# Optimization experiments

Measured on AMD Instinct MI355X. Metric: run time of the kernel, lower is better.

The kernel has to match this reference:

```python
import jax, jax.numpy as jnp
import numpy as np
import math

N_EMBD = 2048
N_HEAD = 16
HEAD_DIM = N_EMBD // N_HEAD  # 128
K = 8
P = 2
B = 1
T = 2048
EPS = 1e-6


def _rms_norm(x):
    return x * jax.lax.rsqrt(jnp.mean(x * x, axis=-1, keepdims=True) + EPS)


def _rope(x, cos, sin):
    # x: [B, T, H, D]; cos/sin: [T, D//2]
    d = x.shape[-1] // 2
    x1, x2 = x[..., :d], x[..., d:]
    c = cos[None, :, None, :]
    s = sin[None, :, None, :]
    return jnp.concatenate([x1 * c + x2 * s, -x1 * s + x2 * c], axis=-1)


def setup_inputs() -> dict:
    key = jax.random.key(0)
    ks = jax.random.split(key, 8)
    x = jax.random.normal(ks[0], (B, T, N_EMBD), jnp.float32)
    half = HEAD_DIM // 2
    inv_freq = 1.0 / (10000.0 ** (np.arange(half, dtype=np.float32) / half))
    ang = np.arange(T, dtype=np.float32)[:, None] * inv_freq[None, :]
    cos = jnp.asarray(np.cos(ang), jnp.float32)
    sin = jnp.asarray(np.sin(ang), jnp.float32)
    sc = 1.0 / math.sqrt(N_EMBD)
    Wq = jax.random.normal(ks[1], (N_EMBD, N_EMBD), jnp.float32) * sc
    Wk = jax.random.normal(ks[2], (N_EMBD, N_EMBD), jnp.float32) * sc
    Wv = jax.random.normal(ks[3], (N_EMBD, N_EMBD), jnp.float32) * sc
    Wproj = jax.random.normal(ks[4], (N_EMBD, N_EMBD), jnp.float32) * sc
    scd = 1.0 / math.sqrt(HEAD_DIM)
    Wdq = jax.random.normal(ks[5], (K, HEAD_DIM), jnp.float32) * scd
    Wdk = jax.random.normal(ks[6], (K, HEAD_DIM), jnp.float32) * scd
    return {"x": x, "cos": cos, "sin": sin, "Wq": Wq, "Wk": Wk, "Wv": Wv, "Wproj": Wproj, "Wdq": Wdq, "Wdk": Wdk}


def reference(x, cos, sin, Wq, Wk, Wv, Wproj, Wdq, Wdk):
    Bq, Tq, C = x.shape
    q = (x @ Wq.T).reshape(Bq, Tq, N_HEAD, HEAD_DIM)
    k = (x @ Wk.T).reshape(Bq, Tq, N_HEAD, HEAD_DIM)
    v = (x @ Wv.T).reshape(Bq, Tq, N_HEAD, HEAD_DIM)
    q = _rms_norm(_rope(q, cos, sin))
    k = _rms_norm(_rope(k, cos, sin))
    q = jnp.swapaxes(q, 1, 2)  # [B,H,T,D]
    k = jnp.swapaxes(k, 1, 2)
    v = jnp.swapaxes(v, 1, 2)
    # base-p digits in {0..p-1}; p=2 -> bits
    qd = jnp.floor(jax.nn.sigmoid(jnp.einsum('bhtd,kd->bhtk', q, Wdq)) * (P - 0.01)).astype(jnp.int32)
    kd = jnp.floor(jax.nn.sigmoid(jnp.einsum('bhtd,kd->bhtk', k, Wdk)) * (P - 0.01)).astype(jnp.int32)
    # lcp >= K-1  <=>  first K-1 digits all equal; pack them into one code
    pw = (P ** jnp.arange(K - 1)).astype(jnp.int32)  # [K-1]
    qc = jnp.sum(qd[..., : K - 1] * pw, axis=-1)  # [B,H,T]
    kc = jnp.sum(kd[..., : K - 1] * pw, axis=-1)
    lcp_mask = qc[..., :, None] == kc[..., None, :]  # [B,H,Tq,Tk]
    causal = jnp.tril(jnp.ones((Tq, Tq), dtype=bool))
    mask = lcp_mask & causal
    scores = jnp.einsum('bhqd,bhkd->bhqk', q, k) * (1.0 / math.sqrt(HEAD_DIM))
    s = jnp.where(mask, scores, -1e30)
    w = jax.nn.softmax(s, axis=-1)
    w = jnp.where(mask, w, 0.0)
    any_valid = jnp.any(mask, axis=-1, keepdims=True)
    w = jnp.where(any_valid, w, 0.0)  # fully-masked rows -> zero output (torch gives NaN)
    y = jnp.einsum('bhqk,bhkd->bhqd', w, v)
    y = jnp.swapaxes(y, 1, 2).reshape(Bq, Tq, C)
    return y @ Wproj.T
```

## Files before the change

### kernel.cpp

```cpp
#include <hip/hip_runtime.h>
#include <hip/hip_bf16.h>
#include <math.h>

#define T 2048
#define C 2048
#define NH 16
#define HD 128
#define SCALE 0.08838834764831845f
#define WL_CAP 2048
#define MARG 1e-4f

typedef short s16x8 __attribute__((ext_vector_type(8)));
typedef float f32x4 __attribute__((ext_vector_type(4)));
typedef _Float16 f16;
typedef f16 f16x8 __attribute__((ext_vector_type(8)));

__device__ __forceinline__ float wave_sum(float v) {
  #pragma unroll
  for (int o = 32; o > 0; o >>= 1) v += __shfl_xor(v, o, 64);
  return v;
}
__device__ __forceinline__ unsigned short f2bf(float f) {
  unsigned u = __float_as_uint(f);
  u += 0x7FFFu + ((u >> 16) & 1u);
  return (unsigned short)(u >> 16);
}

__global__ __launch_bounds__(256) void to_bf16(const float* __restrict__ in,
                                               unsigned short* __restrict__ outp,
                                               int n4) {
  int i = blockIdx.x * blockDim.x + threadIdx.x;
  const int stride = gridDim.x * blockDim.x;
  for (; i < n4; i += stride) {
    float4 v = ((const float4*)in)[i];
    ushort4 o;
    o.x = f2bf(v.x); o.y = f2bf(v.y); o.z = f2bf(v.z); o.w = f2bf(v.w);
    ((ushort4*)outp)[i] = o;
  }
}

#define PRESC 4096.0f
#define S0F 5.9604644775390625e-8f
#define S1F 2.9103830456733704e-11f
#define S2F 1.4210854715202004e-14f

__global__ __launch_bounds__(256) void split_f16(const float* __restrict__ in,
                                                 unsigned short* __restrict__ hip_,
                                                 unsigned short* __restrict__ lop,
                                                 int n4) {
  int i = blockIdx.x * blockDim.x + threadIdx.x;
  const int stride = gridDim.x * blockDim.x;
  for (; i < n4; i += stride) {
    float4 v = ((const float4*)in)[i];
    float s0 = v.x * PRESC, s1 = v.y * PRESC, s2 = v.z * PRESC, s3 = v.w * PRESC;
    union { f16 h[4]; ushort4 u; } H, L;
    H.h[0] = (f16)s0; H.h[1] = (f16)s1; H.h[2] = (f16)s2; H.h[3] = (f16)s3;
    L.h[0] = (f16)((s0 - (float)H.h[0]) * 2048.0f);
    L.h[1] = (f16)((s1 - (float)H.h[1]) * 2048.0f);
    L.h[2] = (f16)((s2 - (float)H.h[2]) * 2048.0f);
    L.h[3] = (f16)((s3 - (float)H.h[3]) * 2048.0f);
    ((ushort4*)hip_)[i] = H.u;
    ((ushort4*)lop)[i] = L.u;
  }
}

#define SBM 64
#define SBN 128
#define SBK 32

__global__ __launch_bounds__(256, 3) void gemm_qk_pre(const unsigned short* __restrict__ Ahp,
                                                      const unsigned short* __restrict__ Alp,
                                                      const unsigned short* __restrict__ Bhp,
                                                      const unsigned short* __restrict__ Blp,
                                                      float* __restrict__ Cc) {
  __shared__ unsigned short Ah[2][SBM * SBK];
  __shared__ unsigned short Av[2][SBM * SBK];
  __shared__ unsigned short Bh[2][SBN * SBK];
  __shared__ unsigned short Bv[2][SBN * SBK];
  const int tid = threadIdx.x;
  const int bm = blockIdx.x * SBM;
  const int bn = blockIdx.y * SBN;
  const int wv = tid >> 6, lane = tid & 63;
  const int wm = wv & 1, wn = wv >> 1;
  const int lrow = lane & 15, lquad = lane >> 4;

  const int a_row = tid >> 2, qg = tid & 3;
  const int a_qs = qg ^ ((a_row >> 1) & 3);
  const int b_row0 = tid >> 2;
  const int b_qs = qg ^ ((b_row0 >> 1) & 3);

  f32x4 acc[2][2][4];
  #pragma unroll
  for (int g = 0; g < 2; ++g)
    #pragma unroll
    for (int i = 0; i < 2; ++i)
      #pragma unroll
      for (int j = 0; j < 4; ++j) acc[g][i][j] = (f32x4){0.f, 0.f, 0.f, 0.f};

  {
    uint4 aH = *(const uint4*)(Ahp + (size_t)(bm + a_row) * C + qg * 8);
    uint4 aL = *(const uint4*)(Alp + (size_t)(bm + a_row) * C + qg * 8);
    uint4 b0H = *(const uint4*)(Bhp + (size_t)(bn + b_row0) * C + qg * 8);
    uint4 b0L = *(const uint4*)(Blp + (size_t)(bn + b_row0) * C + qg * 8);
    uint4 b1H = *(const uint4*)(Bhp + (size_t)(bn + 64 + b_row0) * C + qg * 8);
    uint4 b1L = *(const uint4*)(Blp + (size_t)(bn + 64 + b_row0) * C + qg * 8);
    *(uint4*)&Ah[0][a_row * SBK + a_qs * 8] = aH;
    *(uint4*)&Av[0][a_row * SBK + a_qs * 8] = aL;
    *(uint4*)&Bh[0][b_row0 * SBK + b_qs * 8] = b0H;
    *(uint4*)&Bv[0][b_row0 * SBK + b_qs * 8] = b0L;
    *(uint4*)&Bh[0][(64 + b_row0) * SBK + b_qs * 8] = b1H;
    *(uint4*)&Bv[0][(64 + b_row0) * SBK + b_qs * 8] = b1L;
  }
  __syncthreads();

  const int niter = C / SBK;
  for (int it = 0; it < niter; ++it) {
    const int cur = it & 1;
    const bool has = (it + 1) < niter;
    uint4 aHn, aLn, b0Hn, b0Ln, b1Hn, b1Ln;
    if (has) {
      const int k0 = (it + 1) * SBK;
      aHn = *(const uint4*)(Ahp + (size_t)(bm + a_row) * C + k0 + qg * 8);
      aLn = *(const uint4*)(Alp + (size_t)(bm + a_row) * C + k0 + qg * 8);
      b0Hn = *(const uint4*)(Bhp + (size_t)(bn + b_row0) * C + k0 + qg * 8);
      b0Ln = *(const uint4*)(Blp + (size_t)(bn + b_row0) * C + k0 + qg * 8);
      b1Hn = *(const uint4*)(Bhp + (size_t)(bn + 64 + b_row0) * C + k0 + qg * 8);
      b1Ln = *(const uint4*)(Blp + (size_t)(bn + 64 + b_row0) * C + k0 + qg * 8);
    }
    f16x8 ah[2], av[2], bh[4], bv[4];
    #pragma unroll
    for (int mi = 0; mi < 2; ++mi) {
      const int r = wm * 32 + mi * 16 + lrow;
      const int q = lquad ^ ((r >> 1) & 3);
      ah[mi] = *(const f16x8*)&Ah[cur][r * SBK + q * 8];
      av[mi] = *(const f16x8*)&Av[cur][r * SBK + q * 8];
    }
    #pragma unroll
    for (int ni = 0; ni < 4; ++ni) {
      const int r = wn * 64 + ni * 16 + lrow;
      const int q = lquad ^ ((r >> 1) & 3);
      bh[ni] = *(const f16x8*)&Bh[cur][r * SBK + q * 8];
      bv[ni] = *(const f16x8*)&Bv[cur][r * SBK + q * 8];
    }
    #pragma unroll
    for (int mi = 0; mi < 2; ++mi)
      #pragma unroll
      for (int ni = 0; ni < 4; ++ni) {
        acc[0][mi][ni] = __builtin_amdgcn_mfma_f32_16x16x32_f16(ah[mi], bh[ni], acc[0][mi][ni], 0, 0, 0);
        acc[1][mi][ni] = __builtin_amdgcn_mfma_f32_16x16x32_f16(ah[mi], bv[ni], acc[1][mi][ni], 0, 0, 0);
        acc[1][mi][ni] = __builtin_amdgcn_mfma_f32_16x16x32_f16(av[mi], bh[ni], acc[1][mi][ni], 0, 0, 0);
      }
    if (has) {
      const int nxt = cur ^ 1;
      *(uint4*)&Ah[nxt][a_row * SBK + a_qs * 8] = aHn;
      *(uint4*)&Av[nxt][a_row * SBK + a_qs * 8] = aLn;
      *(uint4*)&Bh[nxt][b_row0 * SBK + b_qs * 8] = b0Hn;
      *(uint4*)&Bv[nxt][b_row0 * SBK + b_qs * 8] = b0Ln;
      *(uint4*)&Bh[nxt][(64 + b_row0) * SBK + b_qs * 8] = b1Hn;
      *(uint4*)&Bv[nxt][(64 + b_row0) * SBK + b_qs * 8] = b1Ln;
    }
    __syncthreads();
  }
  #pragma unroll
  for (int mi = 0; mi < 2; ++mi)
    #pragma unroll
    for (int ni = 0; ni < 4; ++ni)
      #pragma unroll
      for (int r = 0; r < 4; ++r) {
        int row = bm + wm * 32 + mi * 16 + lquad * 4 + r;
        int col = bn + wn * 64 + ni * 16 + lrow;
        Cc[(size_t)row * C + col] = acc[0][mi][ni][r] * S0F + acc[1][mi][ni][r] * S1F;
      }
}

__device__ __forceinline__ void split8(const float4 v0, const float4 v1,
                                       uint4& hi, uint4& lo) {
  float s[8] = {v0.x * PRESC, v0.y * PRESC, v0.z * PRESC, v0.w * PRESC,
                v1.x * PRESC, v1.y * PRESC, v1.z * PRESC, v1.w * PRESC};
  union { uint4 u; f16 h[8]; } H, L;
  #pragma unroll
  for (int i = 0; i < 8; ++i) {
    f16 h2 = (f16)s[i];
    float d = s[i] - (float)h2;
    H.h[i] = h2;
    L.h[i] = (f16)(d * 2048.0f);
  }
  hi = H.u; lo = L.u;
}

__global__ __launch_bounds__(256, 2) void gemm_qk_split16(const float* __restrict__ A,
                                                          const float* __restrict__ Wq,
                                                          const float* __restrict__ Wk,
                                                          float* __restrict__ Qo,
                                                          float* __restrict__ Ko) {
  const float* __restrict__ Bw = blockIdx.z ? Wk : Wq;
  float* __restrict__ Cc = blockIdx.z ? Ko : Qo;
  __shared__ unsigned short Ah[2][SBM * SBK];
  __shared__ unsigned short Av[2][SBM * SBK];
  __shared__ unsigned short Bh[2][SBN * SBK];
  __shared__ unsigned short Bv[2][SBN * SBK];
  const int tid = threadIdx.x;
  const int bm = blockIdx.x * SBM;
  const int bn = blockIdx.y * SBN;
  const int wv = tid >> 6, lane = tid & 63;
  const int wm = wv & 1, wn = wv >> 1;
  const int lrow = lane & 15, lquad = lane >> 4;

  const int a_row = tid >> 2, qg = tid & 3;
  const int a_qs = qg ^ ((a_row >> 1) & 3);
  const int b_row0 = tid >> 2;
  const int b_qs = qg ^ ((b_row0 >> 1) & 3);

  f32x4 acc[3][2][4];
  #pragma unroll
  for (int g = 0; g < 3; ++g)
    #pragma unroll
    for (int i = 0; i < 2; ++i)
      #pragma unroll
      for (int j = 0; j < 4; ++j) acc[g][i][j] = (f32x4){0.f, 0.f, 0.f, 0.f};

  {
    const float* pA  = A  + (size_t)(bm + a_row) * C + qg * 8;
    const float* pB0 = Bw + (size_t)(bn + b_row0) * C + qg * 8;
    const float* pB1 = Bw + (size_t)(bn + 64 + b_row0) * C + qg * 8;
    uint4 h, l;
    split8(*(const float4*)pA, *(const float4*)(pA + 4), h, l);
    *(uint4*)&Ah[0][a_row * SBK + a_qs * 8] = h;
    *(uint4*)&Av[0][a_row * SBK + a_qs * 8] = l;
    split8(*(const float4*)pB0, *(const float4*)(pB0 + 4), h, l);
    *(uint4*)&Bh[0][b_row0 * SBK + b_qs * 8] = h;
    *(uint4*)&Bv[0][b_row0 * SBK + b_qs * 8] = l;
    split8(*(const float4*)pB1, *(const float4*)(pB1 + 4), h, l);
    *(uint4*)&Bh[0][(64 + b_row0) * SBK + b_qs * 8] = h;
    *(uint4*)&Bv[0][(64 + b_row0) * SBK + b_qs * 8] = l;
  }
  __syncthreads();

  const int niter = C / SBK;
  for (int it = 0; it < niter; ++it) {
    const int cur = it & 1;
    const bool has = (it + 1) < niter;
    float4 a0n, a1n, b00n, b01n, b10n, b11n;
    if (has) {
      const int k0 = (it + 1) * SBK;
      const float* pA  = A  + (size_t)(bm + a_row) * C + k0 + qg * 8;
      const float* pB0 = Bw + (size_t)(bn + b_row0) * C + k0 + qg * 8;
      const float* pB1 = Bw + (size_t)(bn + 64 + b_row0) * C + k0 + qg * 8;
      a0n = *(const float4*)pA;   a1n = *(const float4*)(pA + 4);
      b00n = *(const float4*)pB0; b01n = *(const float4*)(pB0 + 4);
      b10n = *(const float4*)pB1; b11n = *(const float4*)(pB1 + 4);
    }
    f16x8 ah[2], av[2], bh[4], bv[4];
    #pragma unroll
    for (int mi = 0; mi < 2; ++mi) {
      const int r = wm * 32 + mi * 16 + lrow;
      const int q = lquad ^ ((r >> 1) & 3);
      ah[mi] = *(const f16x8*)&Ah[cur][r * SBK + q * 8];
      av[mi] = *(const f16x8*)&Av[cur][r * SBK + q * 8];
    }
    #pragma unroll
    for (int ni = 0; ni < 4; ++ni) {
      const int r = wn * 64 + ni * 16 + lrow;
      const int q = lquad ^ ((r >> 1) & 3);
      bh[ni] = *(const f16x8*)&Bh[cur][r * SBK + q * 8];
      bv[ni] = *(const f16x8*)&Bv[cur][r * SBK + q * 8];
    }
    #pragma unroll
    for (int mi = 0; mi < 2; ++mi)
      #pragma unroll
      for (int ni = 0; ni < 4; ++ni) {
        acc[0][mi][ni] = __builtin_amdgcn_mfma_f32_16x16x32_f16(ah[mi], bh[ni], acc[0][mi][ni], 0, 0, 0);
        acc[1][mi][ni] = __builtin_amdgcn_mfma_f32_16x16x32_f16(ah[mi], bv[ni], acc[1][mi][ni], 0, 0, 0);
        acc[1][mi][ni] = __builtin_amdgcn_mfma_f32_16x16x32_f16(av[mi], bh[ni], acc[1][mi][ni], 0, 0, 0);
        acc[2][mi][ni] = __builtin_amdgcn_mfma_f32_16x16x32_f16(av[mi], bv[ni], acc[2][mi][ni], 0, 0, 0);
      }
    if (has) {
      const int nxt = cur ^ 1;
      uint4 h, l;
      split8(a0n, a1n, h, l);
      *(uint4*)&Ah[nxt][a_row * SBK + a_qs * 8] = h;
      *(uint4*)&Av[nxt][a_row * SBK + a_qs * 8] = l;
      split8(b00n, b01n, h, l);
      *(uint4*)&Bh[nxt][b_row0 * SBK + b_qs * 8] = h;
      *(uint4*)&Bv[nxt][b_row0 * SBK + b_qs * 8] = l;
      split8(b10n, b11n, h, l);
      *(uint4*)&Bh[nxt][(64 + b_row0) * SBK + b_qs * 8] = h;
      *(uint4*)&Bv[nxt][(64 + b_row0) * SBK + b_qs * 8] = l;
    }
    __syncthreads();
  }
  #pragma unroll
  for (int mi = 0; mi < 2; ++mi)
    #pragma unroll
    for (int ni = 0; ni < 4; ++ni)
      #pragma unroll
      for (int r = 0; r < 4; ++r) {
        int row = bm + wm * 32 + mi * 16 + lquad * 4 + r;
        int col = bn + wn * 64 + ni * 16 + lrow;
        float v = acc[0][mi][ni][r] * S0F + (acc[1][mi][ni][r] * S1F + acc[2][mi][ni][r] * S2F);
        Cc[(size_t)row * C + col] = v;
      }
}

#define VBM 64
#define VBN 128
#define VBK 32

__global__ __launch_bounds__(256) void gemm_bf16n(const unsigned short* __restrict__ A,
                                                  const unsigned short* __restrict__ B,
                                                  float* __restrict__ Cc) {
  __shared__ unsigned short Al[2][VBM * VBK];
  __shared__ unsigned short Bl[2][VBN * VBK];
  const int tid = threadIdx.x;
  const int bm = blockIdx.x * VBM;
  const int bn = blockIdx.y * VBN;
  const int wv = tid >> 6, lane = tid & 63;
  const int wm = wv & 1, wn = wv >> 1;
  const int lrow = lane & 15, lquad = lane >> 4;

  const int a_row = tid >> 2, qg = tid & 3;
  const int a_qs = qg ^ ((a_row >> 1) & 3);
  const int b_row0 = tid >> 2;
  const int b_qs = qg ^ ((b_row0 >> 1) & 3);

  f32x4 acc[2][4];
  #pragma unroll
  for (int i = 0; i < 2; ++i)
    #pragma unroll
    for (int j = 0; j < 4; ++j) acc[i][j] = (f32x4){0.f, 0.f, 0.f, 0.f};

  {
    uint4 av = *(const uint4*)(A + (size_t)(bm + a_row) * C + qg * 8);
    uint4 b0 = *(const uint4*)(B + (size_t)(bn + b_row0) * C + qg * 8);
    uint4 b1 = *(const uint4*)(B + (size_t)(bn + 64 + b_row0) * C + qg * 8);
    *(uint4*)&Al[0][a_row * VBK + a_qs * 8] = av;
    *(uint4*)&Bl[0][b_row0 * VBK + b_qs * 8] = b0;
    *(uint4*)&Bl[0][(64 + b_row0) * VBK + b_qs * 8] = b1;
  }
  __syncthreads();

  const int niter = C / VBK;
  for (int it = 0; it < niter; ++it) {
    const int cur = it & 1;
    const bool has = (it + 1) < niter;
    uint4 avn, b0n, b1n;
    if (has) {
      const int k0 = (it + 1) * VBK;
      avn = *(const uint4*)(A + (size_t)(bm + a_row) * C + k0 + qg * 8);
      b0n = *(const uint4*)(B + (size_t)(bn + b_row0) * C + k0 + qg * 8);
      b1n = *(const uint4*)(B + (size_t)(bn + 64 + b_row0) * C + k0 + qg * 8);
    }
    s16x8 af[2], bfr[4];
    #pragma unroll
    for (int mi = 0; mi < 2; ++mi) {
      const int r = wm * 32 + mi * 16 + lrow;
      const int q = lquad ^ ((r >> 1) & 3);
      af[mi] = *(const s16x8*)&Al[cur][r * VBK + q * 8];
    }
    #pragma unroll
    for (int ni = 0; ni < 4; ++ni) {
      const int r = wn * 64 + ni * 16 + lrow;
      const int q = lquad ^ ((r >> 1) & 3);
      bfr[ni] = *(const s16x8*)&Bl[cur][r * VBK + q * 8];
    }
    #pragma unroll
    for (int mi = 0; mi < 2; ++mi)
      #pragma unroll
      for (int ni = 0; ni < 4; ++ni)
        acc[mi][ni] = __builtin_amdgcn_mfma_f32_16x16x32_bf16(af[mi], bfr[ni], acc[mi][ni], 0, 0, 0);
    if (has) {
      const int nxt = cur ^ 1;
      *(uint4*)&Al[nxt][a_row * VBK + a_qs * 8] = avn;
      *(uint4*)&Bl[nxt][b_row0 * VBK + b_qs * 8] = b0n;
      *(uint4*)&Bl[nxt][(64 + b_row0) * VBK + b_qs * 8] = b1n;
    }
    __syncthreads();
  }
  #pragma unroll
  for (int mi = 0; mi < 2; ++mi)
    #pragma unroll
    for (int ni = 0; ni < 4; ++ni)
      #pragma unroll
      for (int r = 0; r < 4; ++r) {
        int row = bm + wm * 32 + mi * 16 + lquad * 4 + r;
        int col = bn + wn * 64 + ni * 16 + lrow;
        Cc[(size_t)row * C + col] = acc[mi][ni][r];
      }
}

__global__ void zero_ctr(int* __restrict__ ctr) {
  if (threadIdx.x == 0) ctr[0] = 0;
}

__global__ __launch_bounds__(256) void rope_fused(float* __restrict__ Qb,
                                                  float* __restrict__ Kb,
                                                  const float* __restrict__ cosb,
                                                  const float* __restrict__ sinb,
                                                  const float* __restrict__ Wdq,
                                                  const float* __restrict__ Wdk,
                                                  int* __restrict__ qcodes,
                                                  int* __restrict__ kcodes,
                                                  int* __restrict__ wl,
                                                  int* __restrict__ ctr) {
  float* __restrict__ buf = blockIdx.y ? Kb : Qb;
  const float* __restrict__ Wd = blockIdx.y ? Wdk : Wdq;
  int* __restrict__ codes = blockIdx.y ? kcodes : qcodes;
  int wave = (blockIdx.x << 2) + (threadIdx.x >> 6);
  int lane = threadIdx.x & 63;
  int t = wave / NH, h = wave % NH;
  size_t base = (size_t)t * C + h * HD;
  float x1 = buf[base + lane];
  float x2 = buf[base + lane + 64];
  float c = cosb[t * 64 + lane];
  float s = sinb[t * 64 + lane];
  float r1 = x1 * c + x2 * s;
  float r2 = x2 * c - x1 * s;
  float ss = wave_sum(r1 * r1 + r2 * r2);
  float inv = 1.0f / sqrtf(ss * (1.0f / 128.0f) + 1e-6f);
  r1 *= inv; r2 *= inv;
  buf[base + lane] = r1;
  buf[base + lane + 64] = r2;
  int code = 0;
  bool marg = false;
  #pragma unroll
  for (int kk = 0; kk < 7; ++kk) {
    float z = r1 * Wd[kk * HD + lane] + r2 * Wd[kk * HD + lane + 64];
    z = wave_sum(z);
    float sig = 1.0f / (1.0f + expf(-z));
    float d = sig * 1.99f - 1.0f;
    if (d >= 0.f) code |= (1 << kk);
    marg |= (fabsf(d) < MARG);
  }
  if (lane == 0) {
    codes[h * T + t] = code;
    if (marg) {
      int i = atomicAdd(ctr, 1);
      if (i < WL_CAP) wl[i] = ((int)blockIdx.y << 15) | (h << 11) | t;
    }
  }
}

__global__ __launch_bounds__(64) void fix_codes(const float* __restrict__ x,
                                                const float* __restrict__ Wq,
                                                const float* __restrict__ Wk,
                                                const float* __restrict__ cosb,
                                                const float* __restrict__ sinb,
                                                const float* __restrict__ Wdq,
                                                const float* __restrict__ Wdk,
                                                int* __restrict__ qc,
                                                int* __restrict__ kc,
                                                const int* __restrict__ wl,
                                                const int* __restrict__ ctr) {
  const int n = min(ctr[0], WL_CAP);
  const int lane = threadIdx.x;
  for (int e = blockIdx.x; e < n; e += gridDim.x) {
    const int ent = wl[e];
    const int isK = ent >> 15;
    const int h = (ent >> 11) & 15;
    const int t = ent & 2047;
    const float* __restrict__ W  = isK ? Wk : Wq;
    const float* __restrict__ Wd = isK ? Wdk : Wdq;
    int* __restrict__ codes = isK ? kc : qc;

    const float* xr = x + (size_t)t * C;
    const float* w0 = W + (size_t)(h * HD + lane) * C;
    const float* w1 = W + (size_t)(h * HD + lane + 64) * C;
    float p0[4] = {0.f, 0.f, 0.f, 0.f};
    float p1[4] = {0.f, 0.f, 0.f, 0.f};
    for (int k = 0; k < C; k += 4) {
      float4 xv = *(const float4*)(xr + k);
      float4 a = *(const float4*)(w0 + k);
      float4 b = *(const float4*)(w1 + k);
      p0[0] += xv.x * a.x; p0[1] += xv.y * a.y;
      p0[2] += xv.z * a.z; p0[3] += xv.w * a.w;
      p1[0] += xv.x * b.x; p1[1] += xv.y * b.y;
      p1[2] += xv.z * b.z; p1[3] += xv.w * b.w;
    }
    float x1 = (p0[0] + p0[1]) + (p0[2] + p0[3]);
    float x2 = (p1[0] + p1[1]) + (p1[2] + p1[3]);
    float c = cosb[t * 64 + lane];
    float s = sinb[t * 64 + lane];
    float r1 = x1 * c + x2 * s;
    float r2 = x2 * c - x1 * s;
    float ss = wave_sum(r1 * r1 + r2 * r2);
    float inv = 1.0f / sqrtf(ss * (1.0f / 128.0f) + 1e-6f);
    r1 *= inv; r2 *= inv;
    int code = 0;
    #pragma unroll
    for (int kk = 0; kk < 7; ++kk) {
      float z = r1 * Wd[kk * HD + lane] + r2 * Wd[kk * HD + lane + 64];
      z = wave_sum(z);
      float sig = 1.0f / (1.0f + expf(-z));
      if (sig * 1.99f >= 1.0f) code |= (1 << kk);
    }
    if (lane == 0) codes[h * T + t] = code;
  }
}

__global__ __launch_bounds__(256) void attn_sparse(const float* __restrict__ Q,
                                                   const float* __restrict__ Kn,
                                                   const float* __restrict__ V,
                                                   const int* __restrict__ qc,
                                                   const int* __restrict__ kc,
                                                   float* __restrict__ Y) {
  const int tid = threadIdx.x;
  const int lane = tid & 63;
  const int wave_id = blockIdx.x * 4 + (tid >> 6);
  const int h = wave_id & (NH - 1);
  const int qrow = wave_id >> 4;
  const size_t hb = (size_t)h * HD;

  const float q0 = Q[(size_t)qrow * C + hb + lane];
  const float q1 = Q[(size_t)qrow * C + hb + lane + 64];
  const int qcode = qc[h * T + qrow];
  const int* kch = kc + h * T;

  float m = -1e30f, l = 0.f, acc0 = 0.f, acc1 = 0.f;

  const int nchunks = (qrow >> 6) + 1;
  int kcj = kch[lane];
  for (int ci = 0; ci < nchunks; ++ci) {
    const int j0 = ci << 6;
    const int cur = kcj;
    if (ci + 1 < nchunks) kcj = kch[j0 + 64 + lane];
    unsigned long long mask = __ballot((cur == qcode) && (j0 + lane <= qrow));
    while (mask) {
      const int j = j0 + (__ffsll((long long)mask) - 1);
      mask &= mask - 1;
      const float* kr = Kn + (size_t)j * C + hb;
      const float* vr = V + (size_t)j * C + hb;
      const float k0v = kr[lane], k1v = kr[lane + 64];
      const float v0 = vr[lane], v1 = vr[lane + 64];
      const float s = wave_sum(q0 * k0v + q1 * k1v) * SCALE;
      const float m_new = fmaxf(m, s);
      const float alpha = __expf(m - m_new);
      const float p = __expf(s - m_new);
      l = l * alpha + p;
      acc0 = acc0 * alpha + p * v0;
      acc1 = acc1 * alpha + p * v1;
      m = m_new;
    }
  }
  const float invl = (l > 0.f) ? 1.0f / l : 0.f;
  Y[(size_t)qrow * C + hb + lane] = acc0 * invl;
  Y[(size_t)qrow * C + hb + lane + 64] = acc1 * invl;
}

extern "C" void kernel_launch(void* const* d_in, const int* in_sizes, int n_in,
                              void* d_out, int out_size, void* d_ws, size_t ws_size,
                              hipStream_t stream) {
  (void)in_sizes; (void)n_in; (void)out_size;
  const float* x     = (const float*)d_in[0];
  const float* cosb  = (const float*)d_in[1];
  const float* sinb  = (const float*)d_in[2];
  const float* Wq    = (const float*)d_in[3];
  const float* Wk    = (const float*)d_in[4];
  const float* Wv    = (const float*)d_in[5];
  const float* Wproj = (const float*)d_in[6];
  const float* Wdq   = (const float*)d_in[7];
  const float* Wdk   = (const float*)d_in[8];
  float* out = (float*)d_out;

  const size_t MB = 1024 * 1024;
  char* ws = (char*)d_ws;
  float* Kbuf = (float*)ws;
  float* V    = (float*)(ws + 16 * MB);
  float* Y    = (float*)(ws + 32 * MB);
  unsigned short* Wbf = (unsigned short*)(ws + 48 * MB);
  unsigned short* xbf = (unsigned short*)Y;
  unsigned short* Ybf = (unsigned short*)Kbuf;
  float* Q    = out;

  const int n4 = T * C / 4;

  if (ws_size >= (size_t)64 * MB) {
    unsigned short* xh  = (unsigned short*)Y;
    unsigned short* xl  = xh + (size_t)T * C;
    unsigned short* wqh = (unsigned short*)Kbuf;
    unsigned short* wql = wqh + (size_t)T * C;
    unsigned short* wkh = Wbf;
    unsigned short* wkl = (unsigned short*)(ws + 56 * MB);
    int* qc  = (int*)Wbf;
    int* kc  = qc + NH * T;
    int* ctr = kc + NH * T;
    int* wl  = ctr + 16;

    to_bf16<<<2048, 256, 0, stream>>>(x, xbf, n4);
    to_bf16<<<2048, 256, 0, stream>>>(Wv, Wbf, n4);
    gemm_bf16n<<<dim3(T / VBM, C / VBN), 256, 0, stream>>>(xbf, Wbf, V);
    split_f16<<<2048, 256, 0, stream>>>(x, xh, xl, n4);
    split_f16<<<2048, 256, 0, stream>>>(Wq, wqh, wql, n4);
    split_f16<<<2048, 256, 0, stream>>>(Wk, wkh, wkl, n4);
    gemm_qk_pre<<<dim3(T / SBM, C / SBN), 256, 0, stream>>>(xh, xl, wqh, wql, Q);
    gemm_qk_pre<<<dim3(T / SBM, C / SBN), 256, 0, stream>>>(xh, xl, wkh, wkl, Kbuf);
    zero_ctr<<<1, 64, 0, stream>>>(ctr);
    rope_fused<<<dim3(T * NH / 4, 2), 256, 0, stream>>>(Q, Kbuf, cosb, sinb, Wdq, Wdk, qc, kc, wl, ctr);
    fix_codes<<<256, 64, 0, stream>>>(x, Wq, Wk, cosb, sinb, Wdq, Wdk, qc, kc, wl, ctr);
    attn_sparse<<<T * NH / 4, 256, 0, stream>>>(Q, Kbuf, V, qc, kc, Y);
    to_bf16<<<2048, 256, 0, stream>>>(Y, Ybf, n4);
    to_bf16<<<2048, 256, 0, stream>>>(Wproj, Wbf, n4);
    gemm_bf16n<<<dim3(T / VBM, C / VBN), 256, 0, stream>>>(Ybf, Wbf, out);
  } else {
    int* qc  = (int*)(Wbf + (size_t)T * C);
    int* kc  = qc + NH * T;
    int* ctr = kc + NH * T;
    int* wl  = ctr + 16;

    to_bf16<<<2048, 256, 0, stream>>>(x, xbf, n4);
    to_bf16<<<2048, 256, 0, stream>>>(Wv, Wbf, n4);
    gemm_bf16n<<<dim3(T / VBM, C / VBN), 256, 0, stream>>>(xbf, Wbf, V);
    gemm_qk_split16<<<dim3(T / SBM, C / SBN, 2), 256, 0, stream>>>(x, Wq, Wk, Q, Kbuf);
    zero_ctr<<<1, 64, 0, stream>>>(ctr);
    rope_fused<<<dim3(T * NH / 4, 2), 256, 0, stream>>>(Q, Kbuf, cosb, sinb, Wdq, Wdk, qc, kc, wl, ctr);
    fix_codes<<<256, 64, 0, stream>>>(x, Wq, Wk, cosb, sinb, Wdq, Wdk, qc, kc, wl, ctr);
    attn_sparse<<<T * NH / 4, 256, 0, stream>>>(Q, Kbuf, V, qc, kc, Y);
    to_bf16<<<2048, 256, 0, stream>>>(Y, Ybf, n4);
    to_bf16<<<2048, 256, 0, stream>>>(Wproj, Wbf, n4);
    gemm_bf16n<<<dim3(T / VBM, C / VBN), 256, 0, stream>>>(Ybf, Wbf, out);
  }
}
```

Before: 504.4 us.

## Merge Q/K split GEMMs into one launch and reuse f16 x for V and proj GEMMs

```diff
diff --git a/kernel.cpp b/kernel.cpp
--- a/kernel.cpp
+++ b/kernel.cpp
@@ -64,15 +64,37 @@
   }
 }
 
+__global__ __launch_bounds__(256) void to_f16h(const float* __restrict__ in,
+                                               unsigned short* __restrict__ outp,
+                                               int n4) {
+  int i = blockIdx.x * blockDim.x + threadIdx.x;
+  const int stride = gridDim.x * blockDim.x;
+  for (; i < n4; i += stride) {
+    float4 v = ((const float4*)in)[i];
+    union { f16 h[4]; ushort4 u; } H;
+    H.h[0] = (f16)(v.x * PRESC); H.h[1] = (f16)(v.y * PRESC);
+    H.h[2] = (f16)(v.z * PRESC); H.h[3] = (f16)(v.w * PRESC);
+    ((ushort4*)outp)[i] = H.u;
+  }
+}
+
 #define SBM 64
 #define SBN 128
 #define SBK 32
 
-__global__ __launch_bounds__(256, 3) void gemm_qk_pre(const unsigned short* __restrict__ Ahp,
-                                                      const unsigned short* __restrict__ Alp,
-                                                      const unsigned short* __restrict__ Bhp,
-                                                      const unsigned short* __restrict__ Blp,
-                                                      float* __restrict__ Cc) {
+__global__ __launch_bounds__(256, 3) void gemm_qk2(const unsigned short* __restrict__ xhp,
+                                                   const unsigned short* __restrict__ xlp,
+                                                   const unsigned short* __restrict__ wqh,
+                                                   const unsigned short* __restrict__ wql,
+                                                   const unsigned short* __restrict__ wkh,
+                                                   const unsigned short* __restrict__ wkl,
+                                                   float* __restrict__ Qo,
+                                                   float* __restrict__ Ko) {
+  const unsigned short* __restrict__ Ahp = xhp;
+  const unsigned short* __restrict__ Alp = xlp;
+  const unsigned short* __restrict__ Bhp = blockIdx.z ? wkh : wqh;
+  const unsigned short* __restrict__ Blp = blockIdx.z ? wkl : wql;
+  float* __restrict__ Cc = blockIdx.z ? Ko : Qo;
   __shared__ unsigned short Ah[2][SBM * SBK];
   __shared__ unsigned short Av[2][SBM * SBK];
   __shared__ unsigned short Bh[2][SBN * SBK];
@@ -170,6 +192,88 @@
         int row = bm + wm * 32 + mi * 16 + lquad * 4 + r;
         int col = bn + wn * 64 + ni * 16 + lrow;
         Cc[(size_t)row * C + col] = acc[0][mi][ni][r] * S0F + acc[1][mi][ni][r] * S1F;
+      }
+}
+
+__global__ __launch_bounds__(256) void gemm_h1(const unsigned short* __restrict__ A,
+                                               const unsigned short* __restrict__ B,
+                                               float* __restrict__ Cc) {
+  __shared__ unsigned short Ah[2][SBM * SBK];
+  __shared__ unsigned short Bh[2][SBN * SBK];
+  const int tid = threadIdx.x;
+  const int bm = blockIdx.x * SBM;
+  const int bn = blockIdx.y * SBN;
+  const int wv = tid >> 6, lane = tid & 63;
+  const int wm = wv & 1, wn = wv >> 1;
+  const int lrow = lane & 15, lquad = lane >> 4;
+
+  const int a_row = tid >> 2, qg = tid & 3;
+  const int a_qs = qg ^ ((a_row >> 1) & 3);
+  const int b_row0 = tid >> 2;
+  const int b_qs = qg ^ ((b_row0 >> 1) & 3);
+
+  f32x4 acc[2][4];
+  #pragma unroll
+  for (int i = 0; i < 2; ++i)
+    #pragma unroll
+    for (int j = 0; j < 4; ++j) acc[i][j] = (f32x4){0.f, 0.f, 0.f, 0.f};
+
+  {
+    uint4 av = *(const uint4*)(A + (size_t)(bm + a_row) * C + qg * 8);
+    uint4 b0 = *(const uint4*)(B + (size_t)(bn + b_row0) * C + qg * 8);
+    uint4 b1 = *(const uint4*)(B + (size_t)(bn + 64 + b_row0) * C + qg * 8);
+    *(uint4*)&Ah[0][a_row * SBK + a_qs * 8] = av;
+    *(uint4*)&Bh[0][b_row0 * SBK + b_qs * 8] = b0;
+    *(uint4*)&Bh[0][(64 + b_row0) * SBK + b_qs * 8] = b1;
+  }
+  __syncthreads();
+
+  const int niter = C / SBK;
+  for (int it = 0; it < niter; ++it) {
+    const int cur = it & 1;
+    const bool has = (it + 1) < niter;
+    uint4 avn, b0n, b1n;
+    if (has) {
+      const int k0 = (it + 1) * SBK;
+      avn = *(const uint4*)(A + (size_t)(bm + a_row) * C + k0 + qg * 8);
+      b0n = *(const uint4*)(B + (size_t)(bn + b_row0) * C + k0 + qg * 8);
+      b1n = *(const uint4*)(B + (size_t)(bn + 64 + b_row0) * C + k0 + qg * 8);
+    }
+    f16x8 af[2], bfr[4];
+    #pragma unroll
+    for (int mi = 0; mi < 2; ++mi) {
+      const int r = wm * 32 + mi * 16 + lrow;
+      const int q = lquad ^ ((r >> 1) & 3);
+      af[mi] = *(const f16x8*)&Ah[cur][r * SBK + q * 8];
+    }
+    #pragma unroll
+    for (int ni = 0; ni < 4; ++ni) {
+      const int r = wn * 64 + ni * 16 + lrow;
+      const int q = lquad ^ ((r >> 1) & 3);
+      bfr[ni] = *(const f16x8*)&Bh[cur][r * SBK + q * 8];
+    }
+    #pragma unroll
+    for (int mi = 0; mi < 2; ++mi)
+      #pragma unroll
+      for (int ni = 0; ni < 4; ++ni)
+        acc[mi][ni] = __builtin_amdgcn_mfma_f32_16x16x32_f16(af[mi], bfr[ni], acc[mi][ni], 0, 0, 0);
+    if (has) {
+      const int nxt = cur ^ 1;
+      *(uint4*)&Ah[nxt][a_row * SBK + a_qs * 8] = avn;
+      *(uint4*)&Bh[nxt][b_row0 * SBK + b_qs * 8] = b0n;
+      *(uint4*)&Bh[nxt][(64 + b_row0) * SBK + b_qs * 8] = b1n;
+    }
+    __syncthreads();
+  }
+  #pragma unroll
+  for (int mi = 0; mi < 2; ++mi)
+    #pragma unroll
+    for (int ni = 0; ni < 4; ++ni)
+      #pragma unroll
+      for (int r = 0; r < 4; ++r) {
+        int row = bm + wm * 32 + mi * 16 + lquad * 4 + r;
+        int col = bn + wn * 64 + ni * 16 + lrow;
+        Cc[(size_t)row * C + col] = acc[mi][ni][r] * S0F;
       }
 }
 
@@ -563,44 +667,48 @@
 
   const size_t MB = 1024 * 1024;
   char* ws = (char*)d_ws;
-  float* Kbuf = (float*)ws;
-  float* V    = (float*)(ws + 16 * MB);
-  float* Y    = (float*)(ws + 32 * MB);
-  unsigned short* Wbf = (unsigned short*)(ws + 48 * MB);
-  unsigned short* xbf = (unsigned short*)Y;
-  unsigned short* Ybf = (unsigned short*)Kbuf;
-  float* Q    = out;
-
   const int n4 = T * C / 4;
 
   if (ws_size >= (size_t)64 * MB) {
-    unsigned short* xh  = (unsigned short*)Y;
-    unsigned short* xl  = xh + (size_t)T * C;
-    unsigned short* wqh = (unsigned short*)Kbuf;
-    unsigned short* wql = wqh + (size_t)T * C;
-    unsigned short* wkh = Wbf;
-    unsigned short* wkl = (unsigned short*)(ws + 56 * MB);
-    int* qc  = (int*)Wbf;
+    unsigned short* xh  = (unsigned short*)(ws);
+    unsigned short* xl  = (unsigned short*)(ws + 8 * MB);
+    unsigned short* wqh = (unsigned short*)(ws + 16 * MB);
+    unsigned short* wql = (unsigned short*)(ws + 24 * MB);
+    unsigned short* wkh = (unsigned short*)(ws + 32 * MB);
+    unsigned short* wkl = (unsigned short*)(ws + 40 * MB);
+    float* K = (float*)(ws + 48 * MB);
+    unsigned short* wvh = (unsigned short*)(ws + 16 * MB);
+    float* V = (float*)(ws + 24 * MB);
+    int* qc  = (int*)(ws + 40 * MB);
     int* kc  = qc + NH * T;
     int* ctr = kc + NH * T;
     int* wl  = ctr + 16;
-
-    to_bf16<<<2048, 256, 0, stream>>>(x, xbf, n4);
-    to_bf16<<<2048, 256, 0, stream>>>(Wv, Wbf, n4);
-    gemm_bf16n<<<dim3(T / VBM, C / VBN), 256, 0, stream>>>(xbf, Wbf, V);
+    float* Y = (float*)(ws);
+    unsigned short* yh  = (unsigned short*)(ws + 16 * MB);
+    unsigned short* wph = (unsigned short*)(ws + 24 * MB);
+    float* Q = out;
+
     split_f16<<<2048, 256, 0, stream>>>(x, xh, xl, n4);
     split_f16<<<2048, 256, 0, stream>>>(Wq, wqh, wql, n4);
     split_f16<<<2048, 256, 0, stream>>>(Wk, wkh, wkl, n4);
-    gemm_qk_pre<<<dim3(T / SBM, C / SBN), 256, 0, stream>>>(xh, xl, wqh, wql, Q);
-    gemm_qk_pre<<<dim3(T / SBM, C / SBN), 256, 0, stream>>>(xh, xl, wkh, wkl, Kbuf);
+    gemm_qk2<<<dim3(T / SBM, C / SBN, 2), 256, 0, stream>>>(xh, xl, wqh, wql, wkh, wkl, Q, K);
+    to_f16h<<<2048, 256, 0, stream>>>(Wv, wvh, n4);
+    gemm_h1<<<dim3(T / SBM, C / SBN), 256, 0, stream>>>(xh, wvh, V);
     zero_ctr<<<1, 64, 0, stream>>>(ctr);
-    rope_fused<<<dim3(T * NH / 4, 2), 256, 0, stream>>>(Q, Kbuf, cosb, sinb, Wdq, Wdk, qc, kc, wl, ctr);
+    rope_fused<<<dim3(T * NH / 4, 2), 256, 0, stream>>>(Q, K, cosb, sinb, Wdq, Wdk, qc, kc, wl, ctr);
     fix_codes<<<256, 64, 0, stream>>>(x, Wq, Wk, cosb, sinb, Wdq, Wdk, qc, kc, wl, ctr);
-    attn_sparse<<<T * NH / 4, 256, 0, stream>>>(Q, Kbuf, V, qc, kc, Y);
-    to_bf16<<<2048, 256, 0, stream>>>(Y, Ybf, n4);
-    to_bf16<<<2048, 256, 0, stream>>>(Wproj, Wbf, n4);
-    gemm_bf16n<<<dim3(T / VBM, C / VBN), 256, 0, stream>>>(Ybf, Wbf, out);
+    attn_sparse<<<T * NH / 4, 256, 0, stream>>>(Q, K, V, qc, kc, Y);
+    to_f16h<<<2048, 256, 0, stream>>>(Y, yh, n4);
+    to_f16h<<<2048, 256, 0, stream>>>(Wproj, wph, n4);
+    gemm_h1<<<dim3(T / SBM, C / SBN), 256, 0, stream>>>(yh, wph, out);
   } else {
+    float* Kbuf = (float*)ws;
+    float* V    = (float*)(ws + 16 * MB);
+    float* Y    = (float*)(ws + 32 * MB);
+    unsigned short* Wbf = (unsigned short*)(ws + 48 * MB);
+    unsigned short* xbf = (unsigned short*)Y;
+    unsigned short* Ybf = (unsigned short*)Kbuf;
+    float* Q    = out;
     int* qc  = (int*)(Wbf + (size_t)T * C);
     int* kc  = qc + NH * T;
     int* ctr = kc + NH * T;
```

Result: no change. 502.3 us (-0.4%).
